# Optimization experiments

Measured on AMD Instinct MI355X. Metric: run time of the kernel, lower is better.

Reference implementation:

```python
import jax, jax.numpy as jnp
import numpy as np

N_NODES = 50000


def _gcn_conv(x, src, dst, deg_inv_sqrt, W, b):
    """One PyG-style GCNConv: h = D^{-1/2}(A+I)D^{-1/2} (x W) + b.
    src/dst already include self-loops; deg_inv_sqrt precomputed per node."""
    h = x @ W                                    # [N, out]
    norm = deg_inv_sqrt[src] * deg_inv_sqrt[dst]  # [E]
    msg = h[src] * norm[:, None]                 # gather + scale, [E, out]
    agg = jax.ops.segment_sum(msg, dst, num_segments=N_NODES)
    return agg + b


def setup_inputs() -> dict:
    key = jax.random.key(0)
    k_x, k_e, k0, k1, k2 = jax.random.split(key, 5)
    d_in, d_hid = 64, 64
    x = jax.random.normal(k_x, (N_NODES, d_in), dtype=jnp.float32)
    edge_index = jax.random.randint(k_e, (2, 800000), 0, N_NODES, dtype=jnp.int64)
    # Glorot-ish init for the three layer weights
    s = 1.0 / np.sqrt(d_in)
    W0 = jax.random.uniform(k0, (d_in, d_hid), jnp.float32, -s, s)
    W1 = jax.random.uniform(k1, (d_hid, d_hid), jnp.float32, -s, s)
    W2 = jax.random.uniform(k2, (d_hid, d_hid), jnp.float32, -s, s)
    b0 = jnp.zeros((d_hid,), jnp.float32)
    b1 = jnp.zeros((d_hid,), jnp.float32)
    b2 = jnp.zeros((d_hid,), jnp.float32)
    return {"x": x, "edge_index": edge_index,
            "W0": W0, "b0": b0, "W1": W1, "b1": b1, "W2": W2, "b2": b2}


def reference(x, edge_index, W0, b0, W1, b1, W2, b2):
    # add self-loops once (shared by all layers)
    loop = jnp.arange(N_NODES, dtype=edge_index.dtype)
    src = jnp.concatenate([edge_index[0], loop])
    dst = jnp.concatenate([edge_index[1], loop])
    deg = jax.ops.segment_sum(jnp.ones_like(dst, dtype=x.dtype), dst,
                              num_segments=N_NODES)
    deg_inv_sqrt = jnp.where(deg > 0, jax.lax.rsqrt(deg), 0.0)

    h = _gcn_conv(x, src, dst, deg_inv_sqrt, W0, b0)
    h = jax.nn.relu(h)  # dropout is identity in eval mode
    h = _gcn_conv(h, src, dst, deg_inv_sqrt, W1, b1)
    h = jax.nn.relu(h)
    h = _gcn_conv(h, src, dst, deg_inv_sqrt, W2, b2)
    return h
```

## Files before the change

kernel.cpp:

```cpp
#include <hip/hip_runtime.h>


#define FEAT 64
#define SCAN_B 1024
#define STILE 68

typedef int v4i __attribute__((ext_vector_type(4)));

__global__ void deg_rank_kernel(const int* __restrict__ dst, int* __restrict__ cnt,
                                int* __restrict__ rank, int E4) {
    int i = blockIdx.x * blockDim.x + threadIdx.x;
    if (i < E4) {
        v4i d = __builtin_nontemporal_load(((const v4i*)dst) + i);
        v4i r;
        r[0] = atomicAdd(&cnt[d[0]], 1);
        r[1] = atomicAdd(&cnt[d[1]], 1);
        r[2] = atomicAdd(&cnt[d[2]], 1);
        r[3] = atomicAdd(&cnt[d[3]], 1);
        __builtin_nontemporal_store(r, ((v4i*)rank) + i);
    }
}

__global__ __launch_bounds__(SCAN_B) void scan_partial_kernel(
    const int* __restrict__ cnt, int* __restrict__ rowptr,
    int* __restrict__ bsum, float* __restrict__ dinv, int n) {
    __shared__ int wsum[SCAN_B / 64 + 1];
    const int tid  = threadIdx.x;
    const int lane = tid & 63;
    const int wid  = tid >> 6;
    const int i = blockIdx.x * SCAN_B + tid;

    int vr = (i < n) ? cnt[i] : 0;
    if (i < n) dinv[i] = rsqrtf((float)(1 + vr));
    int v = (vr + 7) & ~7;
    int incl = v;
#pragma unroll
    for (int off = 1; off < 64; off <<= 1) {
        int t = __shfl_up(incl, off, 64);
        if (lane >= off) incl += t;
    }
    if (lane == 63) wsum[wid] = incl;
    __syncthreads();
    if (tid == 0) {
        int run = 0;
#pragma unroll
        for (int w = 0; w < SCAN_B / 64; ++w) { int t = wsum[w]; wsum[w] = run; run += t; }
        wsum[SCAN_B / 64] = run;
        bsum[blockIdx.x] = run;
    }
    __syncthreads();
    if (i < n) rowptr[i] = incl - v + wsum[wid];
}

__global__ __launch_bounds__(SCAN_B) void scan_finish_kernel(
    const int* __restrict__ cnt, int* __restrict__ rowptr,
    const int* __restrict__ bsum, int* __restrict__ col,
    int n, int nb, int dummy) {
    __shared__ int s_off, s_tot;
    const int tid = threadIdx.x;
    if (tid < 64) {
        int v = (tid < nb) ? bsum[tid] : 0;
        int incl = v;
#pragma unroll
        for (int off = 1; off < 64; off <<= 1) {
            int t = __shfl_up(incl, off, 64);
            if ((tid & 63) >= off) incl += t;
        }
        if (tid == (int)blockIdx.x) s_off = incl - v;
        if (tid == 63) s_tot = incl;
    }
    __syncthreads();
    const int i = blockIdx.x * SCAN_B + tid;
    if (i < n) {
        const int rp = rowptr[i] + s_off;
        rowptr[i] = rp;
        const int c = cnt[i];
        const int e = rp + ((c + 7) & ~7);
        for (int p = rp + c; p < e; ++p) col[p] = dummy;
    }
    if (i == 0) rowptr[n] = s_tot;
}

__global__ void scatter_kernel(const int* __restrict__ src, const int* __restrict__ dst,
                               const int* __restrict__ rank, const int* __restrict__ rowptr,
                               int* __restrict__ col, int E4, int qn, int n) {
    const int q = blockIdx.x & 7;
    const int i = (blockIdx.x >> 3) * blockDim.x + threadIdx.x;
    const int nlo = q * qn;
    const int nhi = (nlo + qn < n) ? nlo + qn : n;
    if (i < E4) {
        v4i s = __builtin_nontemporal_load(((const v4i*)src) + i);
        v4i d = __builtin_nontemporal_load(((const v4i*)dst) + i);
        v4i r = __builtin_nontemporal_load(((const v4i*)rank) + i);
#pragma unroll
        for (int j = 0; j < 4; ++j) {
            if (d[j] >= nlo && d[j] < nhi) col[rowptr[d[j]] + r[j]] = s[j];
        }
    }
}

__global__ void prescale_kernel(const float* __restrict__ x, const float* __restrict__ dinv,
                                float* __restrict__ P1, float* __restrict__ P2, int nq) {
    int i = blockIdx.x * blockDim.x + threadIdx.x;
    if (i < nq) {
        float d = dinv[i >> 4];
        float4 v = ((const float4*)x)[i];
        ((float4*)P1)[i] = make_float4(v.x * d, v.y * d, v.z * d, v.w * d);
    } else if (i < nq + 16) {
        const float4 z = make_float4(0.f, 0.f, 0.f, 0.f);
        ((float4*)P1)[i] = z;
        ((float4*)P2)[i] = z;
    }
}

template<int INTER>
__global__ __launch_bounds__(256) void layer_kernel(
    const int* __restrict__ rowptr, const int* __restrict__ col,
    const float* __restrict__ dinv, const float* __restrict__ Xs,
    const float* __restrict__ W, const float* __restrict__ bias,
    float* __restrict__ out, int n) {
    __shared__ float w_lds[FEAT * FEAT];
    __shared__ float s_tile[16 * STILE];

    const int t = threadIdx.x;
#pragma unroll
    for (int i = 0; i < 4; ++i) {
        int idx = (i * 256 + t) * 4;
        *(float4*)&w_lds[idx] = *(const float4*)&W[idx];
    }
    __syncthreads();

    const int r  = t >> 4;
    const int c4 = t & 15;
    const int g  = blockIdx.x * 16 + r;
    if (g >= n) return;
    const int f = c4 * 4;
    const float* __restrict__ Hf = Xs + f;

    float4 a0 = *(const float4*)&Hf[(size_t)g * FEAT];
    float4 a1 = make_float4(0.f, 0.f, 0.f, 0.f);
    float4 a2 = make_float4(0.f, 0.f, 0.f, 0.f);
    float4 a3 = make_float4(0.f, 0.f, 0.f, 0.f);

    int p = rowptr[g];
    const int end = rowptr[g + 1];

    for (; p < end; p += 8) {
        const v4i c0 = *(const v4i*)&col[p];
        const v4i c1 = *(const v4i*)&col[p + 4];
        const float4 h0 = *(const float4*)&Hf[(size_t)c0[0] * FEAT];
        const float4 h1 = *(const float4*)&Hf[(size_t)c0[1] * FEAT];
        const float4 h2 = *(const float4*)&Hf[(size_t)c0[2] * FEAT];
        const float4 h3 = *(const float4*)&Hf[(size_t)c0[3] * FEAT];
        const float4 h4 = *(const float4*)&Hf[(size_t)c1[0] * FEAT];
        const float4 h5 = *(const float4*)&Hf[(size_t)c1[1] * FEAT];
        const float4 h6 = *(const float4*)&Hf[(size_t)c1[2] * FEAT];
        const float4 h7 = *(const float4*)&Hf[(size_t)c1[3] * FEAT];
        a0.x += h0.x; a0.y += h0.y; a0.z += h0.z; a0.w += h0.w;
        a1.x += h1.x; a1.y += h1.y; a1.z += h1.z; a1.w += h1.w;
        a2.x += h2.x; a2.y += h2.y; a2.z += h2.z; a2.w += h2.w;
        a3.x += h3.x; a3.y += h3.y; a3.z += h3.z; a3.w += h3.w;
        a0.x += h4.x; a0.y += h4.y; a0.z += h4.z; a0.w += h4.w;
        a1.x += h5.x; a1.y += h5.y; a1.z += h5.z; a1.w += h5.w;
        a2.x += h6.x; a2.y += h6.y; a2.z += h6.z; a2.w += h6.w;
        a3.x += h7.x; a3.y += h7.y; a3.z += h7.z; a3.w += h7.w;
    }
    float4 S = make_float4((a0.x + a1.x) + (a2.x + a3.x),
                           (a0.y + a1.y) + (a2.y + a3.y),
                           (a0.z + a1.z) + (a2.z + a3.z),
                           (a0.w + a1.w) + (a2.w + a3.w));
    *(float4*)&s_tile[r * STILE + f] = S;

    float4 acc = make_float4(0.f, 0.f, 0.f, 0.f);
#pragma unroll
    for (int k = 0; k < FEAT; ++k) {
        const float sv = s_tile[r * STILE + k];
        const float4 wv = *(const float4*)&w_lds[k * FEAT + f];
        acc.x += sv * wv.x; acc.y += sv * wv.y;
        acc.z += sv * wv.z; acc.w += sv * wv.w;
    }

    const float dg = dinv[g];
    const float4 bv = *(const float4*)&bias[f];
    float4 o = make_float4(acc.x * dg + bv.x, acc.y * dg + bv.y,
                           acc.z * dg + bv.z, acc.w * dg + bv.w);
    if (INTER) {
        o.x = fmaxf(o.x, 0.f) * dg; o.y = fmaxf(o.y, 0.f) * dg;
        o.z = fmaxf(o.z, 0.f) * dg; o.w = fmaxf(o.w, 0.f) * dg;
    }
    *(float4*)&out[(size_t)g * FEAT + f] = o;
}

extern "C" void kernel_launch(void* const* d_in, const int* in_sizes, int n_in,
                              void* d_out, int out_size, void* d_ws, size_t ws_size,
                              hipStream_t stream) {
    const float* x  = (const float*)d_in[0];
    const int*   ei = (const int*)d_in[1];
    const float* W0 = (const float*)d_in[2];
    const float* b0 = (const float*)d_in[3];
    const float* W1 = (const float*)d_in[4];
    const float* b1 = (const float*)d_in[5];
    const float* W2 = (const float*)d_in[6];
    const float* b2 = (const float*)d_in[7];
    float* out = (float*)d_out;

    const int N = in_sizes[0] / FEAT;
    const int E = in_sizes[1] / 2;
    const int* src = ei;
    const int* dst = ei + E;

    const int nbScan = (N + SCAN_B - 1) / SCAN_B;
    const int Ecap = E + 8 * N;

    char* w = (char*)d_ws;
    auto take = [&](size_t bytes) { char* p = w; w += (bytes + 63) & ~(size_t)63; return p; };
    int*   cnt    = (int*)take(sizeof(int) * (size_t)N);
    int*   rowptr = (int*)take(sizeof(int) * (size_t)(N + 1));
    int*   bsum   = (int*)take(sizeof(int) * (size_t)(nbScan + 1));
    int*   col    = (int*)take(sizeof(int) * (size_t)Ecap);
    float* dinv   = (float*)take(sizeof(float) * (size_t)N);
    float* P1     = (float*)take(sizeof(float) * ((size_t)(N + 1) * FEAT));
    float* P2     = (float*)take(sizeof(float) * ((size_t)(N + 1) * FEAT));
    int*   rank = (int*)P2;

    const int tB = 256;
    const int E4  = E / 4;
    const int gE4 = (E4 + tB - 1) / tB;
    const int g16 = (N + 15) / 16;
    const int qn  = (N + 7) / 8;
    const int nq  = N * FEAT / 4;
    const int gQ  = (nq + 16 + tB - 1) / tB;

    hipMemsetAsync(cnt, 0, sizeof(int) * (size_t)N, stream);
    deg_rank_kernel<<<gE4, tB, 0, stream>>>(dst, cnt, rank, E4);
    scan_partial_kernel<<<nbScan, SCAN_B, 0, stream>>>(cnt, rowptr, bsum, dinv, N);
    scan_finish_kernel<<<nbScan, SCAN_B, 0, stream>>>(cnt, rowptr, bsum, col, N, nbScan, N);
    scatter_kernel<<<gE4 * 8, tB, 0, stream>>>(src, dst, rank, rowptr, col, E4, qn, N);

    prescale_kernel<<<gQ, tB, 0, stream>>>(x, dinv, P1, P2, nq);

    layer_kernel<1><<<g16, tB, 0, stream>>>(rowptr, col, dinv, P1, W0, b0, P2, N);
    layer_kernel<1><<<g16, tB, 0, stream>>>(rowptr, col, dinv, P2, W1, b1, P1, N);
    layer_kernel<0><<<g16, tB, 0, stream>>>(rowptr, col, dinv, P1, W2, b2, out, N);
}
```

Before: 232.1 us.

## Split aggregation from GEMM and partition feature columns across XCDs

Splits each fused layer kernel into a separate gather-aggregation kernel and a GEMM kernel, joined by an intermediate AGG buffer. The aggregation kernel uses blockIdx modulo 8 to place each 16-float feature quarter on its own XCD pair, so each XCD's L2 only has to hold a quarter of the feature matrix for the random gathers. It also uses a persistent grid-stride loop and nontemporal loads and stores. The cost is an extra write and read of the N×64 aggregate per layer, three more kernel launches, and reliance on the round-robin mapping of blocks to XCDs.

```diff
diff --git a/kernel.cpp b/kernel.cpp
--- a/kernel.cpp
+++ b/kernel.cpp
@@ -5,7 +5,8 @@
 #define SCAN_B 1024
 #define STILE 68
 
-typedef int v4i __attribute__((ext_vector_type(4)));
+typedef int   v4i __attribute__((ext_vector_type(4)));
+typedef float v4f __attribute__((ext_vector_type(4)));
 
 __global__ void deg_rank_kernel(const int* __restrict__ dst, int* __restrict__ cnt,
                                 int* __restrict__ rank, int E4) {
@@ -113,10 +114,65 @@
     }
 }
 
+__global__ __launch_bounds__(256) void agg_kernel(
+    const int* __restrict__ rowptr, const int* __restrict__ col,
+    const float* __restrict__ Xs, float* __restrict__ AGG,
+    int n, int NG, int HG, int BPH) {
+    const int xcd  = blockIdx.x & 7;
+    const int q    = xcd & 3;
+    const int half = xcd >> 2;
+    const int j    = blockIdx.x >> 3;
+    const int t  = threadIdx.x;
+    const int rl = t >> 2;
+    const int l  = t & 3;
+    const int fq = q * 16 + l * 4;
+    const float* __restrict__ Hf = Xs + fq;
+
+    const int gi_end = ((half + 1) * HG < NG) ? (half + 1) * HG : NG;
+    for (int gi = half * HG + j; gi < gi_end; gi += BPH) {
+        const int g = gi * 64 + rl;
+        if (g >= n) continue;
+
+        float4 a0 = *(const float4*)&Hf[(size_t)g * FEAT];
+        float4 a1 = make_float4(0.f, 0.f, 0.f, 0.f);
+        float4 a2 = make_float4(0.f, 0.f, 0.f, 0.f);
+        float4 a3 = make_float4(0.f, 0.f, 0.f, 0.f);
+
+        int p = rowptr[g];
+        const int end = rowptr[g + 1];
+
+        for (; p < end; p += 8) {
+            const v4i c0 = __builtin_nontemporal_load((const v4i*)&col[p]);
+            const v4i c1 = __builtin_nontemporal_load((const v4i*)&col[p + 4]);
+            const float4 h0 = *(const float4*)&Hf[(size_t)c0[0] * FEAT];
+            const float4 h1 = *(const float4*)&Hf[(size_t)c0[1] * FEAT];
+            const float4 h2 = *(const float4*)&Hf[(size_t)c0[2] * FEAT];
+            const float4 h3 = *(const float4*)&Hf[(size_t)c0[3] * FEAT];
+            const float4 h4 = *(const float4*)&Hf[(size_t)c1[0] * FEAT];
+            const float4 h5 = *(const float4*)&Hf[(size_t)c1[1] * FEAT];
+            const float4 h6 = *(const float4*)&Hf[(size_t)c1[2] * FEAT];
+            const float4 h7 = *(const float4*)&Hf[(size_t)c1[3] * FEAT];
+            a0.x += h0.x; a0.y += h0.y; a0.z += h0.z; a0.w += h0.w;
+            a1.x += h1.x; a1.y += h1.y; a1.z += h1.z; a1.w += h1.w;
+            a2.x += h2.x; a2.y += h2.y; a2.z += h2.z; a2.w += h2.w;
+            a3.x += h3.x; a3.y += h3.y; a3.z += h3.z; a3.w += h3.w;
+            a0.x += h4.x; a0.y += h4.y; a0.z += h4.z; a0.w += h4.w;
+            a1.x += h5.x; a1.y += h5.y; a1.z += h5.z; a1.w += h5.w;
+            a2.x += h6.x; a2.y += h6.y; a2.z += h6.z; a2.w += h6.w;
+            a3.x += h7.x; a3.y += h7.y; a3.z += h7.z; a3.w += h7.w;
+        }
+        v4f S;
+        S.x = (a0.x + a1.x) + (a2.x + a3.x);
+        S.y = (a0.y + a1.y) + (a2.y + a3.y);
+        S.z = (a0.z + a1.z) + (a2.z + a3.z);
+        S.w = (a0.w + a1.w) + (a2.w + a3.w);
+        __builtin_nontemporal_store(S, (v4f*)&AGG[(size_t)g * FEAT + fq]);
+    }
+}
+
 template<int INTER>
-__global__ __launch_bounds__(256) void layer_kernel(
-    const int* __restrict__ rowptr, const int* __restrict__ col,
-    const float* __restrict__ dinv, const float* __restrict__ Xs,
+__global__ __launch_bounds__(256) void gemm_kernel(
+    const float* __restrict__ AGG, const float* __restrict__ dinv,
     const float* __restrict__ W, const float* __restrict__ bias,
     float* __restrict__ out, int n) {
     __shared__ float w_lds[FEAT * FEAT];
@@ -135,41 +191,9 @@
     const int g  = blockIdx.x * 16 + r;
     if (g >= n) return;
     const int f = c4 * 4;
-    const float* __restrict__ Hf = Xs + f;
-
-    float4 a0 = *(const float4*)&Hf[(size_t)g * FEAT];
-    float4 a1 = make_float4(0.f, 0.f, 0.f, 0.f);
-    float4 a2 = make_float4(0.f, 0.f, 0.f, 0.f);
-    float4 a3 = make_float4(0.f, 0.f, 0.f, 0.f);
-
-    int p = rowptr[g];
-    const int end = rowptr[g + 1];
-
-    for (; p < end; p += 8) {
-        const v4i c0 = *(const v4i*)&col[p];
-        const v4i c1 = *(const v4i*)&col[p + 4];
-        const float4 h0 = *(const float4*)&Hf[(size_t)c0[0] * FEAT];
-        const float4 h1 = *(const float4*)&Hf[(size_t)c0[1] * FEAT];
-        const float4 h2 = *(const float4*)&Hf[(size_t)c0[2] * FEAT];
-        const float4 h3 = *(const float4*)&Hf[(size_t)c0[3] * FEAT];
-        const float4 h4 = *(const float4*)&Hf[(size_t)c1[0] * FEAT];
-        const float4 h5 = *(const float4*)&Hf[(size_t)c1[1] * FEAT];
-        const float4 h6 = *(const float4*)&Hf[(size_t)c1[2] * FEAT];
-        const float4 h7 = *(const float4*)&Hf[(size_t)c1[3] * FEAT];
-        a0.x += h0.x; a0.y += h0.y; a0.z += h0.z; a0.w += h0.w;
-        a1.x += h1.x; a1.y += h1.y; a1.z += h1.z; a1.w += h1.w;
-        a2.x += h2.x; a2.y += h2.y; a2.z += h2.z; a2.w += h2.w;
-        a3.x += h3.x; a3.y += h3.y; a3.z += h3.z; a3.w += h3.w;
-        a0.x += h4.x; a0.y += h4.y; a0.z += h4.z; a0.w += h4.w;
-        a1.x += h5.x; a1.y += h5.y; a1.z += h5.z; a1.w += h5.w;
-        a2.x += h6.x; a2.y += h6.y; a2.z += h6.z; a2.w += h6.w;
-        a3.x += h7.x; a3.y += h7.y; a3.z += h7.z; a3.w += h7.w;
-    }
-    float4 S = make_float4((a0.x + a1.x) + (a2.x + a3.x),
-                           (a0.y + a1.y) + (a2.y + a3.y),
-                           (a0.z + a1.z) + (a2.z + a3.z),
-                           (a0.w + a1.w) + (a2.w + a3.w));
-    *(float4*)&s_tile[r * STILE + f] = S;
+
+    const v4f S = __builtin_nontemporal_load((const v4f*)&AGG[(size_t)g * FEAT + f]);
+    *(v4f*)&s_tile[r * STILE + f] = S;
 
     float4 acc = make_float4(0.f, 0.f, 0.f, 0.f);
 #pragma unroll
@@ -221,7 +245,8 @@
     float* dinv   = (float*)take(sizeof(float) * (size_t)N);
     float* P1     = (float*)take(sizeof(float) * ((size_t)(N + 1) * FEAT));
     float* P2     = (float*)take(sizeof(float) * ((size_t)(N + 1) * FEAT));
-    int*   rank = (int*)P2;
+    float* AGG    = (float*)take(sizeof(float) * ((size_t)N * FEAT));
+    int*   rank = (int*)AGG;
 
     const int tB = 256;
     const int E4  = E / 4;
@@ -231,6 +256,11 @@
     const int nq  = N * FEAT / 4;
     const int gQ  = (nq + 16 + tB - 1) / tB;
 
+    const int NG  = (N + 63) / 64;
+    const int HG  = (NG + 1) / 2;
+    const int BPH = 192;
+    const int gAgg = 8 * BPH;
+
     hipMemsetAsync(cnt, 0, sizeof(int) * (size_t)N, stream);
     deg_rank_kernel<<<gE4, tB, 0, stream>>>(dst, cnt, rank, E4);
     scan_partial_kernel<<<nbScan, SCAN_B, 0, stream>>>(cnt, rowptr, bsum, dinv, N);
@@ -239,7 +269,10 @@
 
     prescale_kernel<<<gQ, tB, 0, stream>>>(x, dinv, P1, P2, nq);
 
-    layer_kernel<1><<<g16, tB, 0, stream>>>(rowptr, col, dinv, P1, W0, b0, P2, N);
-    layer_kernel<1><<<g16, tB, 0, stream>>>(rowptr, col, dinv, P2, W1, b1, P1, N);
-    layer_kernel<0><<<g16, tB, 0, stream>>>(rowptr, col, dinv, P1, W2, b2, out, N);
-}
+    agg_kernel<<<gAgg, tB, 0, stream>>>(rowptr, col, P1, AGG, N, NG, HG, BPH);
+    gemm_kernel<1><<<g16, tB, 0, stream>>>(AGG, dinv, W0, b0, P2, N);
+    agg_kernel<<<gAgg, tB, 0, stream>>>(rowptr, col, P2, AGG, N, NG, HG, BPH);
+    gemm_kernel<1><<<g16, tB, 0, stream>>>(AGG, dinv, W1, b1, P1, N);
+    agg_kernel<<<gAgg, tB, 0, stream>>>(rowptr, col, P1, AGG, N, NG, HG, BPH);
+    gemm_kernel<0><<<g16, tB, 0, stream>>>(AGG, dinv, W2, b2, out, N);
+}
```

After: 314.6 us. 35.6% more time.
